# Kernel optimization log

Measured on AMD Instinct MI355X. Metric: run time of the kernel, lower is better.

## Reference

```python
import jax, jax.numpy as jnp
import numpy as np

N, E, IN, H, D = 20000, 640000, 256, 4, 32
NEG_SLOPE = 0.2


def setup_inputs() -> dict:
    key = jax.random.key(0)
    ks = jax.random.split(key, 8)
    feat = jax.random.normal(ks[0], (N, IN), dtype=jnp.float32)
    pr_score = jax.random.uniform(ks[1], (N,), dtype=jnp.float32) + 1e-3
    edge_src = jax.random.randint(ks[2], (E,), 0, N)
    edge_dst = jax.random.randint(ks[3], (E,), 0, N)
    # parameters (xavier-ish scale)
    fc_w = jax.random.normal(ks[4], (H * D, IN), dtype=jnp.float32) * (2.0 / np.sqrt(IN + H * D))
    attn_l = jax.random.normal(ks[5], (1, H, D), dtype=jnp.float32) * (2.0 / np.sqrt(1 + D))
    attn_r = jax.random.normal(ks[6], (1, H, D), dtype=jnp.float32) * (2.0 / np.sqrt(1 + D))
    bias = jnp.zeros((H * D,), dtype=jnp.float32)
    return {"feat": feat, "pr_score": pr_score, "edge_src": edge_src,
            "edge_dst": edge_dst, "fc_w": fc_w, "attn_l": attn_l,
            "attn_r": attn_r, "bias": bias}


def reference(feat, pr_score, edge_src, edge_dst, fc_w, attn_l, attn_r, bias):
    n = feat.shape[0]
    h, d = attn_l.shape[1], attn_l.shape[2]
    # feat_src = fc(feat).view(N, H, D)
    ft = (feat @ fc_w.T).reshape(n, h, d)                       # [N,H,D]
    el = jnp.sum(ft * attn_l, axis=-1)                          # [N,H]
    er = jnp.sum(ft * attn_r, axis=-1)                          # [N,H]
    e = jax.nn.leaky_relu(el[edge_src] + er[edge_dst], NEG_SLOPE)  # [E,H]
    # edge_softmax over incoming edges per destination node
    emax = jax.ops.segment_max(e, edge_dst, num_segments=n)
    ee = jnp.exp(e - emax[edge_dst])
    esum = jax.ops.segment_sum(ee, edge_dst, num_segments=n)
    a = ee / esum[edge_dst]                                     # [E,H]
    # PageRank-style normalization: b = pr[src] / sum_{in-edges}(pr[src])
    pr_src = pr_score[edge_src]                                 # [E]
    pr_sum = jax.ops.segment_sum(pr_src, edge_dst, num_segments=n)
    b = pr_src / pr_sum[edge_dst]                               # [E]
    c = a * b[:, None]                                          # [E,H]
    csum = jax.ops.segment_sum(c, edge_dst, num_segments=n)
    c = c / csum[edge_dst]                                      # [E,H]
    # weighted aggregation: rst[dst] = sum_e ft[src_e] * c_e
    m = ft[edge_src] * c[:, :, None]                            # [E,H,D]
    rst = jax.ops.segment_sum(m, edge_dst, num_segments=n)      # [N,H,D]
    rst = rst + bias.reshape(1, h, d)
    return rst
```

## Files before the change

kernel.cpp:

```cpp
#include <hip/hip_runtime.h>

#define IN_DIM 256
#define HD 128
#define NHEAD 4
#define NEG_SLOPE 0.2f
#define ELLW 128

typedef unsigned int  uint;
typedef unsigned short ushort_t;

typedef short bf16x8 __attribute__((ext_vector_type(8)));
typedef float f32x4  __attribute__((ext_vector_type(4)));

__device__ __forceinline__ ushort_t f2bf(float x) {
    uint u = __float_as_uint(x);
    u += 0x7fffu + ((u >> 16) & 1u);
    return (ushort_t)(u >> 16);
}
__device__ __forceinline__ uint pack2(float lo, float hi) {
    return (uint)f2bf(lo) | ((uint)f2bf(hi) << 16);
}
__device__ __forceinline__ float bflo(uint u) { return __uint_as_float(u << 16); }
__device__ __forceinline__ float bfhi(uint u) { return __uint_as_float(u & 0xffff0000u); }

#define GBM 64
#define GBK 64
#define LDK 72

__global__ __launch_bounds__(256) void gemm_mfma(
    const float* __restrict__ feat, const float* __restrict__ fcw,
    const float* __restrict__ attn_l, const float* __restrict__ attn_r,
    const float* __restrict__ pr,
    ushort_t* __restrict__ ft16, float* __restrict__ elp, float* __restrict__ er,
    int* __restrict__ deg, int n)
{
    __shared__ ushort_t s_a[GBM * LDK];
    __shared__ ushort_t s_b[64 * LDK];

    const int t = threadIdx.x;
    {
        const int z = blockIdx.x * 256 + t;
        if (z < n) deg[z] = 0;
    }

    const int tile = blockIdx.x >> 1;
    const int half = blockIdx.x & 1;
    const int row0 = tile * GBM;
    const int col0 = half * 64;
    const int w    = t >> 6;
    const int lane = t & 63;
    const int fr   = lane & 15;
    const int fq   = lane >> 4;

    f32x4 acc[4];
#pragma unroll
    for (int nt = 0; nt < 4; ++nt) acc[nt] = (f32x4){0.f, 0.f, 0.f, 0.f};

    const int s_row = t >> 2, s_kca = (t & 3) * 16;
    const int s_col = t >> 2, s_kcb = (t & 3) * 16;

    const ushort_t* pa  = &s_a[(w * 16 + fr) * LDK + fq * 8];
    const ushort_t* pb0 = &s_b[fr * LDK + fq * 8];

    for (int k0 = 0; k0 < IN_DIM; k0 += GBK) {
        {
            const int grow = row0 + s_row;
            float4 v0, v1, v2, v3;
            if (grow < n) {
                const float* p = feat + (size_t)grow * IN_DIM + k0 + s_kca;
                v0 = *(const float4*)(p + 0);
                v1 = *(const float4*)(p + 4);
                v2 = *(const float4*)(p + 8);
                v3 = *(const float4*)(p + 12);
            } else {
                v0 = make_float4(0.f,0.f,0.f,0.f); v1 = v0; v2 = v0; v3 = v0;
            }
            uint4* dst = (uint4*)&s_a[s_row * LDK + s_kca];
            dst[0] = make_uint4(pack2(v0.x,v0.y), pack2(v0.z,v0.w),
                                pack2(v1.x,v1.y), pack2(v1.z,v1.w));
            dst[1] = make_uint4(pack2(v2.x,v2.y), pack2(v2.z,v2.w),
                                pack2(v3.x,v3.y), pack2(v3.z,v3.w));
        }
        {
            const float* p = fcw + (size_t)(col0 + s_col) * IN_DIM + k0 + s_kcb;
            float4 u0 = *(const float4*)(p + 0);
            float4 u1 = *(const float4*)(p + 4);
            float4 u2 = *(const float4*)(p + 8);
            float4 u3 = *(const float4*)(p + 12);
            uint4* dst = (uint4*)&s_b[s_col * LDK + s_kcb];
            dst[0] = make_uint4(pack2(u0.x,u0.y), pack2(u0.z,u0.w),
                                pack2(u1.x,u1.y), pack2(u1.z,u1.w));
            dst[1] = make_uint4(pack2(u2.x,u2.y), pack2(u2.z,u2.w),
                                pack2(u3.x,u3.y), pack2(u3.z,u3.w));
        }
        __syncthreads();

        const bf16x8 a0 = *(const bf16x8*)pa;
        const bf16x8 a1 = *(const bf16x8*)(pa + 32);
#pragma unroll
        for (int nt = 0; nt < 4; ++nt) {
            const ushort_t* pb = pb0 + nt * 16 * LDK;
            const bf16x8 b0 = *(const bf16x8*)pb;
            const bf16x8 b1 = *(const bf16x8*)(pb + 32);
            acc[nt] = __builtin_amdgcn_mfma_f32_16x16x32_bf16(a0, b0, acc[nt], 0, 0, 0);
            acc[nt] = __builtin_amdgcn_mfma_f32_16x16x32_bf16(a1, b1, acc[nt], 0, 0, 0);
        }
        __syncthreads();
    }

    const int h0 = 2 * half;
    float al[4], ar_[4];
#pragma unroll
    for (int nt = 0; nt < 4; ++nt) {
        al[nt]  = attn_l[col0 + nt * 16 + fr];
        ar_[nt] = attn_r[col0 + nt * 16 + fr];
    }

#pragma unroll
    for (int j = 0; j < 4; ++j) {
        const int grow = row0 + w * 16 + fq * 4 + j;
        const bool ok = grow < n;
        if (ok) {
#pragma unroll
            for (int nt = 0; nt < 4; ++nt)
                ft16[(size_t)grow * HD + col0 + nt * 16 + fr] = f2bf(acc[nt][j]);
        }
        float plA = acc[0][j]*al[0] + acc[1][j]*al[1];
        float plB = acc[2][j]*al[2] + acc[3][j]*al[3];
        float peA = acc[0][j]*ar_[0] + acc[1][j]*ar_[1];
        float peB = acc[2][j]*ar_[2] + acc[3][j]*ar_[3];
#pragma unroll
        for (int m = 1; m < 16; m <<= 1) {
            plA += __shfl_xor(plA, m, 64); plB += __shfl_xor(plB, m, 64);
            peA += __shfl_xor(peA, m, 64); peB += __shfl_xor(peB, m, 64);
        }
        if (ok && fr == 0) {
            *(float2*)&elp[(size_t)grow * 8 + h0] = make_float2(plA, plB);
            *(float2*)&er[(size_t)grow * NHEAD + h0] = make_float2(peA, peB);
            if (half == 0) elp[(size_t)grow * 8 + 4] = pr[grow];
        }
    }
}

__global__ void build_ell(const int* __restrict__ src, const int* __restrict__ dst,
                          int* __restrict__ deg, int* __restrict__ ell, int e)
{
    int i = blockIdx.x * blockDim.x + threadIdx.x;
    if (i < e) {
        const int d = dst[i];
        const int r = atomicAdd(&deg[d], 1);
        if (r < ELLW) ell[(size_t)d * ELLW + r] = src[i];
    }
}

__global__ __launch_bounds__(256) void aggregate(
    const uint4* __restrict__ ftu4, const float* __restrict__ elp,
    const float* __restrict__ er,
    const int* __restrict__ deg, const int* __restrict__ ell,
    const float* __restrict__ bias, float* __restrict__ out, int n)
{
    const int wave = threadIdx.x >> 6;
    const int lane = threadIdx.x & 63;
    const int slot = lane >> 4;
    const int sub  = lane & 15;
    const int head = sub >> 2;
    const int dst  = blockIdx.x * 4 + wave;

    __shared__ float s_w[4][NHEAD][72];
    __shared__ int   s_s[4][72];

    if (dst >= n) return;

    if (lane < 8) {
        s_s[wave][64 + lane] = 0;
#pragma unroll
        for (int hh = 0; hh < NHEAD; ++hh) s_w[wave][hh][64 + lane] = 0.f;
    }

    const int dg  = min(deg[dst], ELLW);
    const int beg = dst * ELLW;
    const float4 e4 = *(const float4*)&er[(size_t)dst * NHEAD];

    float aA[8], aB[8];
#pragma unroll
    for (int i = 0; i < 8; ++i) { aA[i] = 0.f; aB[i] = 0.f; }
    float wS = 0.f;

    for (int base = 0; base < dg; base += 64) {
        const int len = min(64, dg - base);
        if (lane < len) {
            const int s = ell[beg + base + lane];
            const float4 l4 = *(const float4*)&elp[(size_t)s * 8];
            const float p   = elp[(size_t)s * 8 + 4];
            float e0 = l4.x + e4.x, e1 = l4.y + e4.y;
            float e2 = l4.z + e4.z, e3 = l4.w + e4.w;
            e0 = e0 > 0.f ? e0 : NEG_SLOPE * e0;
            e1 = e1 > 0.f ? e1 : NEG_SLOPE * e1;
            e2 = e2 > 0.f ? e2 : NEG_SLOPE * e2;
            e3 = e3 > 0.f ? e3 : NEG_SLOPE * e3;
            s_w[wave][0][lane] = __expf(e0) * p;
            s_w[wave][1][lane] = __expf(e1) * p;
            s_w[wave][2][lane] = __expf(e2) * p;
            s_w[wave][3][lane] = __expf(e3) * p;
            s_s[wave][lane] = s;
        } else {
            s_w[wave][0][lane] = 0.f; s_w[wave][1][lane] = 0.f;
            s_w[wave][2][lane] = 0.f; s_w[wave][3][lane] = 0.f;
            s_s[wave][lane] = 0;
        }
        for (int j = 0; j < len; j += 8) {
            const int eA = j + slot;
            const int eB = j + 4 + slot;
            const int   sA = s_s[wave][eA];
            const int   sB = s_s[wave][eB];
            const float wA = s_w[wave][head][eA];
            const float wB = s_w[wave][head][eB];
            const uint4 uA = ftu4[(size_t)sA * 16 + sub];
            const uint4 uB = ftu4[(size_t)sB * 16 + sub];
            wS += wA + wB;
            aA[0] = fmaf(wA, bflo(uA.x), aA[0]);
            aA[1] = fmaf(wA, bfhi(uA.x), aA[1]);
            aA[2] = fmaf(wA, bflo(uA.y), aA[2]);
            aA[3] = fmaf(wA, bfhi(uA.y), aA[3]);
            aA[4] = fmaf(wA, bflo(uA.z), aA[4]);
            aA[5] = fmaf(wA, bfhi(uA.z), aA[5]);
            aA[6] = fmaf(wA, bflo(uA.w), aA[6]);
            aA[7] = fmaf(wA, bfhi(uA.w), aA[7]);
            aB[0] = fmaf(wB, bflo(uB.x), aB[0]);
            aB[1] = fmaf(wB, bfhi(uB.x), aB[1]);
            aB[2] = fmaf(wB, bflo(uB.y), aB[2]);
            aB[3] = fmaf(wB, bfhi(uB.y), aB[3]);
            aB[4] = fmaf(wB, bflo(uB.z), aB[4]);
            aB[5] = fmaf(wB, bfhi(uB.z), aB[5]);
            aB[6] = fmaf(wB, bflo(uB.w), aB[6]);
            aB[7] = fmaf(wB, bfhi(uB.w), aB[7]);
        }
    }

    float a[8];
#pragma unroll
    for (int i = 0; i < 8; ++i) a[i] = aA[i] + aB[i];
#pragma unroll
    for (int i = 0; i < 8; ++i) {
        a[i] += __shfl_xor(a[i], 16, 64);
        a[i] += __shfl_xor(a[i], 32, 64);
    }
    wS += __shfl_xor(wS, 16, 64);
    wS += __shfl_xor(wS, 32, 64);

    if (slot == 0) {
        const float inv = (dg > 0) ? 1.f / wS : 0.f;
        const float4 b0 = *(const float4*)&bias[8 * sub];
        const float4 b1 = *(const float4*)&bias[8 * sub + 4];
        float4 r0, r1;
        r0.x = a[0] * inv + b0.x; r0.y = a[1] * inv + b0.y;
        r0.z = a[2] * inv + b0.z; r0.w = a[3] * inv + b0.w;
        r1.x = a[4] * inv + b1.x; r1.y = a[5] * inv + b1.y;
        r1.z = a[6] * inv + b1.z; r1.w = a[7] * inv + b1.w;
        *(float4*)&out[(size_t)dst * HD + 8 * sub]     = r0;
        *(float4*)&out[(size_t)dst * HD + 8 * sub + 4] = r1;
    }
}

extern "C" void kernel_launch(void* const* d_in, const int* in_sizes, int n_in,
                              void* d_out, int out_size, void* d_ws, size_t ws_size,
                              hipStream_t stream)
{
    const float* feat   = (const float*)d_in[0];
    const float* pr     = (const float*)d_in[1];
    const int*   esrc   = (const int*)d_in[2];
    const int*   edst   = (const int*)d_in[3];
    const float* fcw    = (const float*)d_in[4];
    const float* attn_l = (const float*)d_in[5];
    const float* attn_r = (const float*)d_in[6];
    const float* bias   = (const float*)d_in[7];
    float* out = (float*)d_out;

    const int n = in_sizes[0] / IN_DIM;
    const int e = in_sizes[2];

    char* ws = (char*)d_ws;
    size_t off = 0;
    auto wsalloc = [&](size_t bytes) -> void* {
        void* p = ws + off;
        off += (bytes + 255) & ~(size_t)255;
        return p;
    };
    ushort_t* ft16 = (ushort_t*)wsalloc((size_t)n * HD * sizeof(ushort_t));
    float* elp  = (float*)wsalloc((size_t)n * 8 * sizeof(float));
    float* er   = (float*)wsalloc((size_t)n * NHEAD * sizeof(float));
    int*   deg  = (int*)wsalloc((size_t)n * sizeof(int));
    int*   ell  = (int*)wsalloc((size_t)n * ELLW * sizeof(int));

    const int ntiles = (n + GBM - 1) / GBM;
    gemm_mfma<<<2 * ntiles, 256, 0, stream>>>(feat, fcw, attn_l, attn_r, pr,
                                              ft16, elp, er, deg, n);
    build_ell<<<(e + 255) / 256, 256, 0, stream>>>(esrc, edst, deg, ell, e);
    aggregate<<<(n + 3) / 4, 256, 0, stream>>>((const uint4*)ft16, elp, er,
                                               deg, ell, bias, out, n);
}
```

Before: 74.36 us.

## Fuse GEMM, ELL build and aggregation into one cooperative persistent kernel

```diff
diff --git a/kernel.cpp b/kernel.cpp
--- a/kernel.cpp
+++ b/kernel.cpp
@@ -1,10 +1,18 @@
 #include <hip/hip_runtime.h>
+#include <hip/hip_cooperative_groups.h>
+
+namespace cg = cooperative_groups;
 
 #define IN_DIM 256
 #define HD 128
 #define NHEAD 4
 #define NEG_SLOPE 0.2f
 #define ELLW 128
+#define GBM 64
+#define GBK 64
+#define LDK 72
+#define GRIDF 512
+#define G_GEMM 352
 
 typedef unsigned int  uint;
 typedef unsigned short ushort_t;
@@ -23,28 +31,17 @@
 __device__ __forceinline__ float bflo(uint u) { return __uint_as_float(u << 16); }
 __device__ __forceinline__ float bfhi(uint u) { return __uint_as_float(u & 0xffff0000u); }
 
-#define GBM 64
-#define GBK 64
-#define LDK 72
-
-__global__ __launch_bounds__(256) void gemm_mfma(
+__device__ __forceinline__ void gemm_half(
+    ushort_t* __restrict__ s_a, ushort_t* __restrict__ s_b, int tile2,
     const float* __restrict__ feat, const float* __restrict__ fcw,
     const float* __restrict__ attn_l, const float* __restrict__ attn_r,
     const float* __restrict__ pr,
     ushort_t* __restrict__ ft16, float* __restrict__ elp, float* __restrict__ er,
-    int* __restrict__ deg, int n)
-{
-    __shared__ ushort_t s_a[GBM * LDK];
-    __shared__ ushort_t s_b[64 * LDK];
-
-    const int t = threadIdx.x;
-    {
-        const int z = blockIdx.x * 256 + t;
-        if (z < n) deg[z] = 0;
-    }
-
-    const int tile = blockIdx.x >> 1;
-    const int half = blockIdx.x & 1;
+    int n)
+{
+    const int t    = threadIdx.x;
+    const int tile = tile2 >> 1;
+    const int half = tile2 & 1;
     const int row0 = tile * GBM;
     const int col0 = half * 64;
     const int w    = t >> 6;
@@ -56,8 +53,7 @@
 #pragma unroll
     for (int nt = 0; nt < 4; ++nt) acc[nt] = (f32x4){0.f, 0.f, 0.f, 0.f};
 
-    const int s_row = t >> 2, s_kca = (t & 3) * 16;
-    const int s_col = t >> 2, s_kcb = (t & 3) * 16;
+    const int s_row = t >> 2, s_kc = (t & 3) * 16;
 
     const ushort_t* pa  = &s_a[(w * 16 + fr) * LDK + fq * 8];
     const ushort_t* pb0 = &s_b[fr * LDK + fq * 8];
@@ -67,7 +63,7 @@
             const int grow = row0 + s_row;
             float4 v0, v1, v2, v3;
             if (grow < n) {
-                const float* p = feat + (size_t)grow * IN_DIM + k0 + s_kca;
+                const float* p = feat + (size_t)grow * IN_DIM + k0 + s_kc;
                 v0 = *(const float4*)(p + 0);
                 v1 = *(const float4*)(p + 4);
                 v2 = *(const float4*)(p + 8);
@@ -75,19 +71,19 @@
             } else {
                 v0 = make_float4(0.f,0.f,0.f,0.f); v1 = v0; v2 = v0; v3 = v0;
             }
-            uint4* dst = (uint4*)&s_a[s_row * LDK + s_kca];
+            uint4* dst = (uint4*)&s_a[s_row * LDK + s_kc];
             dst[0] = make_uint4(pack2(v0.x,v0.y), pack2(v0.z,v0.w),
                                 pack2(v1.x,v1.y), pack2(v1.z,v1.w));
             dst[1] = make_uint4(pack2(v2.x,v2.y), pack2(v2.z,v2.w),
                                 pack2(v3.x,v3.y), pack2(v3.z,v3.w));
         }
         {
-            const float* p = fcw + (size_t)(col0 + s_col) * IN_DIM + k0 + s_kcb;
+            const float* p = fcw + (size_t)(col0 + s_row) * IN_DIM + k0 + s_kc;
             float4 u0 = *(const float4*)(p + 0);
             float4 u1 = *(const float4*)(p + 4);
             float4 u2 = *(const float4*)(p + 8);
             float4 u3 = *(const float4*)(p + 12);
-            uint4* dst = (uint4*)&s_b[s_col * LDK + s_kcb];
+            uint4* dst = (uint4*)&s_b[s_row * LDK + s_kc];
             dst[0] = make_uint4(pack2(u0.x,u0.y), pack2(u0.z,u0.w),
                                 pack2(u1.x,u1.y), pack2(u1.z,u1.w));
             dst[1] = make_uint4(pack2(u2.x,u2.y), pack2(u2.z,u2.w),
@@ -142,40 +138,16 @@
     }
 }
 
-__global__ void build_ell(const int* __restrict__ src, const int* __restrict__ dst,
-                          int* __restrict__ deg, int* __restrict__ ell, int e)
-{
-    int i = blockIdx.x * blockDim.x + threadIdx.x;
-    if (i < e) {
-        const int d = dst[i];
-        const int r = atomicAdd(&deg[d], 1);
-        if (r < ELLW) ell[(size_t)d * ELLW + r] = src[i];
-    }
-}
-
-__global__ __launch_bounds__(256) void aggregate(
+__device__ __forceinline__ void agg_one(
     const uint4* __restrict__ ftu4, const float* __restrict__ elp,
     const float* __restrict__ er,
     const int* __restrict__ deg, const int* __restrict__ ell,
-    const float* __restrict__ bias, float* __restrict__ out, int n)
-{
-    const int wave = threadIdx.x >> 6;
-    const int lane = threadIdx.x & 63;
+    const float* __restrict__ bias, float* __restrict__ out,
+    int dst, int lane, float (*__restrict__ sw)[72], int* __restrict__ ss)
+{
     const int slot = lane >> 4;
     const int sub  = lane & 15;
     const int head = sub >> 2;
-    const int dst  = blockIdx.x * 4 + wave;
-
-    __shared__ float s_w[4][NHEAD][72];
-    __shared__ int   s_s[4][72];
-
-    if (dst >= n) return;
-
-    if (lane < 8) {
-        s_s[wave][64 + lane] = 0;
-#pragma unroll
-        for (int hh = 0; hh < NHEAD; ++hh) s_w[wave][hh][64 + lane] = 0.f;
-    }
 
     const int dg  = min(deg[dst], ELLW);
     const int beg = dst * ELLW;
@@ -198,23 +170,23 @@
             e1 = e1 > 0.f ? e1 : NEG_SLOPE * e1;
             e2 = e2 > 0.f ? e2 : NEG_SLOPE * e2;
             e3 = e3 > 0.f ? e3 : NEG_SLOPE * e3;
-            s_w[wave][0][lane] = __expf(e0) * p;
-            s_w[wave][1][lane] = __expf(e1) * p;
-            s_w[wave][2][lane] = __expf(e2) * p;
-            s_w[wave][3][lane] = __expf(e3) * p;
-            s_s[wave][lane] = s;
+            sw[0][lane] = __expf(e0) * p;
+            sw[1][lane] = __expf(e1) * p;
+            sw[2][lane] = __expf(e2) * p;
+            sw[3][lane] = __expf(e3) * p;
+            ss[lane] = s;
         } else {
-            s_w[wave][0][lane] = 0.f; s_w[wave][1][lane] = 0.f;
-            s_w[wave][2][lane] = 0.f; s_w[wave][3][lane] = 0.f;
-            s_s[wave][lane] = 0;
+            sw[0][lane] = 0.f; sw[1][lane] = 0.f;
+            sw[2][lane] = 0.f; sw[3][lane] = 0.f;
+            ss[lane] = 0;
         }
         for (int j = 0; j < len; j += 8) {
             const int eA = j + slot;
             const int eB = j + 4 + slot;
-            const int   sA = s_s[wave][eA];
-            const int   sB = s_s[wave][eB];
-            const float wA = s_w[wave][head][eA];
-            const float wB = s_w[wave][head][eB];
+            const int   sA = ss[eA];
+            const int   sB = ss[eB];
+            const float wA = sw[head][eA];
+            const float wB = sw[head][eB];
             const uint4 uA = ftu4[(size_t)sA * 16 + sub];
             const uint4 uB = ftu4[(size_t)sB * 16 + sub];
             wS += wA + wB;
@@ -262,6 +234,106 @@
     }
 }
 
+union SmemU {
+    struct { ushort_t a[GBM * LDK]; ushort_t b[64 * LDK]; } g;
+    struct { float w[4][NHEAD][72]; int s[4][72]; } agg;
+};
+
+__global__ void
+__attribute__((amdgpu_flat_work_group_size(256, 256), amdgpu_waves_per_eu(2, 2)))
+fused_all(
+    const float* __restrict__ feat, const float* __restrict__ pr,
+    const int* __restrict__ esrc, const int* __restrict__ edst,
+    const float* __restrict__ fcw, const float* __restrict__ attn_l,
+    const float* __restrict__ attn_r, const float* __restrict__ bias,
+    float* __restrict__ out, ushort_t* __restrict__ ft16,
+    float* __restrict__ elp, float* __restrict__ er,
+    int* __restrict__ deg, int* __restrict__ ell, int n, int e)
+{
+    __shared__ SmemU sm;
+    const int t = threadIdx.x;
+    cg::grid_group grid = cg::this_grid();
+
+    for (int i = blockIdx.x * 256 + t; i < n; i += GRIDF * 256) deg[i] = 0;
+    __threadfence();
+    grid.sync();
+
+    if (blockIdx.x < G_GEMM) {
+        const int ntiles2 = 2 * ((n + GBM - 1) / GBM);
+        for (int t2 = blockIdx.x; t2 < ntiles2; t2 += G_GEMM)
+            gemm_half(sm.g.a, sm.g.b, t2, feat, fcw, attn_l, attn_r, pr,
+                      ft16, elp, er, n);
+    } else {
+        const int stride = (GRIDF - G_GEMM) * 256;
+        for (int i = (blockIdx.x - G_GEMM) * 256 + t; i < e; i += stride) {
+            const int d = edst[i];
+            const int r = atomicAdd(&deg[d], 1);
+            if (r < ELLW) ell[(size_t)d * ELLW + r] = esrc[i];
+        }
+    }
+    __threadfence();
+    grid.sync();
+
+    const int wave = t >> 6;
+    const int lane = t & 63;
+    float (*sw)[72] = sm.agg.w[wave];
+    int* ss = sm.agg.s[wave];
+    if (lane < 8) {
+        ss[64 + lane] = 0;
+#pragma unroll
+        for (int hh = 0; hh < NHEAD; ++hh) sw[hh][64 + lane] = 0.f;
+    }
+    for (int dst = blockIdx.x * 4 + wave; dst < n; dst += GRIDF * 4)
+        agg_one((const uint4*)ft16, elp, er, deg, ell, bias, out,
+                dst, lane, sw, ss);
+}
+
+__global__ __launch_bounds__(256) void gemm_mfma_k(
+    const float* __restrict__ feat, const float* __restrict__ fcw,
+    const float* __restrict__ attn_l, const float* __restrict__ attn_r,
+    const float* __restrict__ pr,
+    ushort_t* __restrict__ ft16, float* __restrict__ elp, float* __restrict__ er,
+    int* __restrict__ deg, int n)
+{
+    __shared__ SmemU sm;
+    const int z = blockIdx.x * 256 + threadIdx.x;
+    if (z < n) deg[z] = 0;
+    gemm_half(sm.g.a, sm.g.b, blockIdx.x, feat, fcw, attn_l, attn_r, pr,
+              ft16, elp, er, n);
+}
+
+__global__ void build_ell_k(const int* __restrict__ src, const int* __restrict__ dst,
+                            int* __restrict__ deg, int* __restrict__ ell, int e)
+{
+    int i = blockIdx.x * blockDim.x + threadIdx.x;
+    if (i < e) {
+        const int d = dst[i];
+        const int r = atomicAdd(&deg[d], 1);
+        if (r < ELLW) ell[(size_t)d * ELLW + r] = src[i];
+    }
+}
+
+__global__ __launch_bounds__(256) void aggregate_k(
+    const uint4* __restrict__ ftu4, const float* __restrict__ elp,
+    const float* __restrict__ er,
+    const int* __restrict__ deg, const int* __restrict__ ell,
+    const float* __restrict__ bias, float* __restrict__ out, int n)
+{
+    __shared__ SmemU sm;
+    const int wave = threadIdx.x >> 6;
+    const int lane = threadIdx.x & 63;
+    float (*sw)[72] = sm.agg.w[wave];
+    int* ss = sm.agg.s[wave];
+    if (lane < 8) {
+        ss[64 + lane] = 0;
+#pragma unroll
+        for (int hh = 0; hh < NHEAD; ++hh) sw[hh][64 + lane] = 0.f;
+    }
+    const int dst = blockIdx.x * 4 + wave;
+    if (dst < n)
+        agg_one(ftu4, elp, er, deg, ell, bias, out, dst, lane, sw, ss);
+}
+
 extern "C" void kernel_launch(void* const* d_in, const int* in_sizes, int n_in,
                               void* d_out, int out_size, void* d_ws, size_t ws_size,
                               hipStream_t stream)
@@ -276,8 +348,8 @@
     const float* bias   = (const float*)d_in[7];
     float* out = (float*)d_out;
 
-    const int n = in_sizes[0] / IN_DIM;
-    const int e = in_sizes[2];
+    int n = in_sizes[0] / IN_DIM;
+    int e = in_sizes[2];
 
     char* ws = (char*)d_ws;
     size_t off = 0;
@@ -292,10 +364,17 @@
     int*   deg  = (int*)wsalloc((size_t)n * sizeof(int));
     int*   ell  = (int*)wsalloc((size_t)n * ELLW * sizeof(int));
 
-    const int ntiles = (n + GBM - 1) / GBM;
-    gemm_mfma<<<2 * ntiles, 256, 0, stream>>>(feat, fcw, attn_l, attn_r, pr,
-                                              ft16, elp, er, deg, n);
-    build_ell<<<(e + 255) / 256, 256, 0, stream>>>(esrc, edst, deg, ell, e);
-    aggregate<<<(n + 3) / 4, 256, 0, stream>>>((const uint4*)ft16, elp, er,
-                                               deg, ell, bias, out, n);
-}
+    void* args[] = { &feat, &pr, &esrc, &edst, &fcw, &attn_l, &attn_r, &bias,
+                     &out, &ft16, &elp, &er, &deg, &ell, &n, &e };
+    hipError_t cerr = hipLaunchCooperativeKernel(fused_all, dim3(GRIDF), dim3(256),
+                                                 args, 0, stream);
+    if (cerr != hipSuccess) {
+        (void)hipGetLastError();
+        const int ntiles2 = 2 * ((n + GBM - 1) / GBM);
+        gemm_mfma_k<<<ntiles2, 256, 0, stream>>>(feat, fcw, attn_l, attn_r, pr,
+                                                 ft16, elp, er, deg, n);
+        build_ell_k<<<(e + 255) / 256, 256, 0, stream>>>(esrc, edst, deg, ell, e);
+        aggregate_k<<<(n + 3) / 4, 256, 0, stream>>>((const uint4*)ft16, elp, er,
+                                                     deg, ell, bias, out, n);
+    }
+}
```

New measurement: 268.3 us. 261% more time.

## Compute edge attention weights in ELL build kernel instead of aggregate

Applied to the files above, without the earlier changes.

```diff
diff --git a/kernel.cpp b/kernel.cpp
--- a/kernel.cpp
+++ b/kernel.cpp
@@ -56,8 +56,7 @@
 #pragma unroll
     for (int nt = 0; nt < 4; ++nt) acc[nt] = (f32x4){0.f, 0.f, 0.f, 0.f};
 
-    const int s_row = t >> 2, s_kca = (t & 3) * 16;
-    const int s_col = t >> 2, s_kcb = (t & 3) * 16;
+    const int s_row = t >> 2, s_kc = (t & 3) * 16;
 
     const ushort_t* pa  = &s_a[(w * 16 + fr) * LDK + fq * 8];
     const ushort_t* pb0 = &s_b[fr * LDK + fq * 8];
@@ -67,7 +66,7 @@
             const int grow = row0 + s_row;
             float4 v0, v1, v2, v3;
             if (grow < n) {
-                const float* p = feat + (size_t)grow * IN_DIM + k0 + s_kca;
+                const float* p = feat + (size_t)grow * IN_DIM + k0 + s_kc;
                 v0 = *(const float4*)(p + 0);
                 v1 = *(const float4*)(p + 4);
                 v2 = *(const float4*)(p + 8);
@@ -75,19 +74,19 @@
             } else {
                 v0 = make_float4(0.f,0.f,0.f,0.f); v1 = v0; v2 = v0; v3 = v0;
             }
-            uint4* dst = (uint4*)&s_a[s_row * LDK + s_kca];
+            uint4* dst = (uint4*)&s_a[s_row * LDK + s_kc];
             dst[0] = make_uint4(pack2(v0.x,v0.y), pack2(v0.z,v0.w),
                                 pack2(v1.x,v1.y), pack2(v1.z,v1.w));
             dst[1] = make_uint4(pack2(v2.x,v2.y), pack2(v2.z,v2.w),
                                 pack2(v3.x,v3.y), pack2(v3.z,v3.w));
         }
         {
-            const float* p = fcw + (size_t)(col0 + s_col) * IN_DIM + k0 + s_kcb;
+            const float* p = fcw + (size_t)(col0 + s_row) * IN_DIM + k0 + s_kc;
             float4 u0 = *(const float4*)(p + 0);
             float4 u1 = *(const float4*)(p + 4);
             float4 u2 = *(const float4*)(p + 8);
             float4 u3 = *(const float4*)(p + 12);
-            uint4* dst = (uint4*)&s_b[s_col * LDK + s_kcb];
+            uint4* dst = (uint4*)&s_b[s_row * LDK + s_kc];
             dst[0] = make_uint4(pack2(u0.x,u0.y), pack2(u0.z,u0.w),
                                 pack2(u1.x,u1.y), pack2(u1.z,u1.w));
             dst[1] = make_uint4(pack2(u2.x,u2.y), pack2(u2.z,u2.w),
@@ -142,21 +141,42 @@
     }
 }
 
-__global__ void build_ell(const int* __restrict__ src, const int* __restrict__ dst,
-                          int* __restrict__ deg, int* __restrict__ ell, int e)
+__global__ void build_ell_w(
+    const int* __restrict__ src, const int* __restrict__ dst,
+    const float* __restrict__ elp, const float* __restrict__ er,
+    int* __restrict__ deg, int* __restrict__ ell_src,
+    float4* __restrict__ ell_w, int e)
 {
     int i = blockIdx.x * blockDim.x + threadIdx.x;
-    if (i < e) {
-        const int d = dst[i];
-        const int r = atomicAdd(&deg[d], 1);
-        if (r < ELLW) ell[(size_t)d * ELLW + r] = src[i];
-    }
+    if (i >= e) return;
+    const int d = dst[i];
+    const int s = src[i];
+    const int r = atomicAdd(&deg[d], 1);
+    if (r >= ELLW) return;
+
+    const float4 l4 = *(const float4*)&elp[(size_t)s * 8];
+    const float p   = elp[(size_t)s * 8 + 4];
+    const float4 e4 = *(const float4*)&er[(size_t)d * NHEAD];
+    float e0 = l4.x + e4.x, e1 = l4.y + e4.y;
+    float e2 = l4.z + e4.z, e3 = l4.w + e4.w;
+    e0 = e0 > 0.f ? e0 : NEG_SLOPE * e0;
+    e1 = e1 > 0.f ? e1 : NEG_SLOPE * e1;
+    e2 = e2 > 0.f ? e2 : NEG_SLOPE * e2;
+    e3 = e3 > 0.f ? e3 : NEG_SLOPE * e3;
+    float4 w4;
+    w4.x = __expf(e0) * p;
+    w4.y = __expf(e1) * p;
+    w4.z = __expf(e2) * p;
+    w4.w = __expf(e3) * p;
+    const size_t slot = (size_t)d * ELLW + r;
+    ell_src[slot] = s;
+    ell_w[slot]   = w4;
 }
 
 __global__ __launch_bounds__(256) void aggregate(
-    const uint4* __restrict__ ftu4, const float* __restrict__ elp,
-    const float* __restrict__ er,
-    const int* __restrict__ deg, const int* __restrict__ ell,
+    const uint4* __restrict__ ftu4,
+    const int* __restrict__ deg, const int* __restrict__ ell_src,
+    const float4* __restrict__ ell_w,
     const float* __restrict__ bias, float* __restrict__ out, int n)
 {
     const int wave = threadIdx.x >> 6;
@@ -179,7 +199,6 @@
 
     const int dg  = min(deg[dst], ELLW);
     const int beg = dst * ELLW;
-    const float4 e4 = *(const float4*)&er[(size_t)dst * NHEAD];
 
     float aA[8], aB[8];
 #pragma unroll
@@ -189,19 +208,10 @@
     for (int base = 0; base < dg; base += 64) {
         const int len = min(64, dg - base);
         if (lane < len) {
-            const int s = ell[beg + base + lane];
-            const float4 l4 = *(const float4*)&elp[(size_t)s * 8];
-            const float p   = elp[(size_t)s * 8 + 4];
-            float e0 = l4.x + e4.x, e1 = l4.y + e4.y;
-            float e2 = l4.z + e4.z, e3 = l4.w + e4.w;
-            e0 = e0 > 0.f ? e0 : NEG_SLOPE * e0;
-            e1 = e1 > 0.f ? e1 : NEG_SLOPE * e1;
-            e2 = e2 > 0.f ? e2 : NEG_SLOPE * e2;
-            e3 = e3 > 0.f ? e3 : NEG_SLOPE * e3;
-            s_w[wave][0][lane] = __expf(e0) * p;
-            s_w[wave][1][lane] = __expf(e1) * p;
-            s_w[wave][2][lane] = __expf(e2) * p;
-            s_w[wave][3][lane] = __expf(e3) * p;
+            const int   s  = ell_src[beg + base + lane];
+            const float4 w4 = ell_w[beg + base + lane];
+            s_w[wave][0][lane] = w4.x; s_w[wave][1][lane] = w4.y;
+            s_w[wave][2][lane] = w4.z; s_w[wave][3][lane] = w4.w;
             s_s[wave][lane] = s;
         } else {
             s_w[wave][0][lane] = 0.f; s_w[wave][1][lane] = 0.f;
@@ -286,16 +296,18 @@
         off += (bytes + 255) & ~(size_t)255;
         return p;
     };
-    ushort_t* ft16 = (ushort_t*)wsalloc((size_t)n * HD * sizeof(ushort_t));
-    float* elp  = (float*)wsalloc((size_t)n * 8 * sizeof(float));
-    float* er   = (float*)wsalloc((size_t)n * NHEAD * sizeof(float));
-    int*   deg  = (int*)wsalloc((size_t)n * sizeof(int));
-    int*   ell  = (int*)wsalloc((size_t)n * ELLW * sizeof(int));
-
-    const int ntiles = (n + GBM - 1) / GBM;
-    gemm_mfma<<<2 * ntiles, 256, 0, stream>>>(feat, fcw, attn_l, attn_r, pr,
-                                              ft16, elp, er, deg, n);
-    build_ell<<<(e + 255) / 256, 256, 0, stream>>>(esrc, edst, deg, ell, e);
-    aggregate<<<(n + 3) / 4, 256, 0, stream>>>((const uint4*)ft16, elp, er,
-                                               deg, ell, bias, out, n);
-}
+    ushort_t* ft16   = (ushort_t*)wsalloc((size_t)n * HD * sizeof(ushort_t));
+    float*    elp    = (float*)wsalloc((size_t)n * 8 * sizeof(float));
+    float*    er     = (float*)wsalloc((size_t)n * NHEAD * sizeof(float));
+    int*      deg    = (int*)wsalloc((size_t)n * sizeof(int));
+    int*      ellsrc = (int*)wsalloc((size_t)n * ELLW * sizeof(int));
+    float4*   ellw   = (float4*)wsalloc((size_t)n * ELLW * sizeof(float4));
+
+    const int ntiles2 = 2 * ((n + GBM - 1) / GBM);
+    gemm_mfma<<<ntiles2, 256, 0, stream>>>(feat, fcw, attn_l, attn_r, pr,
+                                           ft16, elp, er, deg, n);
+    build_ell_w<<<(e + 255) / 256, 256, 0, stream>>>(esrc, edst, elp, er,
+                                                     deg, ellsrc, ellw, e);
+    aggregate<<<(n + 3) / 4, 256, 0, stream>>>((const uint4*)ft16,
+                                               deg, ellsrc, ellw, bias, out, n);
+}
```

New measurement: 78.80 us. +6.0%, slower.

## Run ELL build concurrently with GEMM in one fused launch

Applied to the files above, without the earlier changes.

```diff
diff --git a/kernel.cpp b/kernel.cpp
--- a/kernel.cpp
+++ b/kernel.cpp
@@ -27,21 +27,35 @@
 #define GBK 64
 #define LDK 72
 
-__global__ __launch_bounds__(256) void gemm_mfma(
+__global__ void zero_deg(int* __restrict__ deg, int n)
+{
+    int i = blockIdx.x * blockDim.x + threadIdx.x;
+    if (i < n) deg[i] = 0;
+}
+
+__global__ __launch_bounds__(256) void gemm_and_ell(
     const float* __restrict__ feat, const float* __restrict__ fcw,
     const float* __restrict__ attn_l, const float* __restrict__ attn_r,
     const float* __restrict__ pr,
+    const int* __restrict__ esrc, const int* __restrict__ edst,
     ushort_t* __restrict__ ft16, float* __restrict__ elp, float* __restrict__ er,
-    int* __restrict__ deg, int n)
+    int* __restrict__ deg, int* __restrict__ ell,
+    int n, int e, int ntiles2)
 {
+    const int t = threadIdx.x;
+
+    if (blockIdx.x >= ntiles2) {
+        const int i = (blockIdx.x - ntiles2) * 256 + t;
+        if (i < e) {
+            const int d = edst[i];
+            const int r = atomicAdd(&deg[d], 1);
+            if (r < ELLW) ell[(size_t)d * ELLW + r] = esrc[i];
+        }
+        return;
+    }
+
     __shared__ ushort_t s_a[GBM * LDK];
     __shared__ ushort_t s_b[64 * LDK];
-
-    const int t = threadIdx.x;
-    {
-        const int z = blockIdx.x * 256 + t;
-        if (z < n) deg[z] = 0;
-    }
 
     const int tile = blockIdx.x >> 1;
     const int half = blockIdx.x & 1;
@@ -56,8 +70,7 @@
 #pragma unroll
     for (int nt = 0; nt < 4; ++nt) acc[nt] = (f32x4){0.f, 0.f, 0.f, 0.f};
 
-    const int s_row = t >> 2, s_kca = (t & 3) * 16;
-    const int s_col = t >> 2, s_kcb = (t & 3) * 16;
+    const int s_row = t >> 2, s_kc = (t & 3) * 16;
 
     const ushort_t* pa  = &s_a[(w * 16 + fr) * LDK + fq * 8];
     const ushort_t* pb0 = &s_b[fr * LDK + fq * 8];
@@ -67,7 +80,7 @@
             const int grow = row0 + s_row;
             float4 v0, v1, v2, v3;
             if (grow < n) {
-                const float* p = feat + (size_t)grow * IN_DIM + k0 + s_kca;
+                const float* p = feat + (size_t)grow * IN_DIM + k0 + s_kc;
                 v0 = *(const float4*)(p + 0);
                 v1 = *(const float4*)(p + 4);
                 v2 = *(const float4*)(p + 8);
@@ -75,19 +88,19 @@
             } else {
                 v0 = make_float4(0.f,0.f,0.f,0.f); v1 = v0; v2 = v0; v3 = v0;
             }
-            uint4* dst = (uint4*)&s_a[s_row * LDK + s_kca];
+            uint4* dst = (uint4*)&s_a[s_row * LDK + s_kc];
             dst[0] = make_uint4(pack2(v0.x,v0.y), pack2(v0.z,v0.w),
                                 pack2(v1.x,v1.y), pack2(v1.z,v1.w));
             dst[1] = make_uint4(pack2(v2.x,v2.y), pack2(v2.z,v2.w),
                                 pack2(v3.x,v3.y), pack2(v3.z,v3.w));
         }
         {
-            const float* p = fcw + (size_t)(col0 + s_col) * IN_DIM + k0 + s_kcb;
+            const float* p = fcw + (size_t)(col0 + s_row) * IN_DIM + k0 + s_kc;
             float4 u0 = *(const float4*)(p + 0);
             float4 u1 = *(const float4*)(p + 4);
             float4 u2 = *(const float4*)(p + 8);
             float4 u3 = *(const float4*)(p + 12);
-            uint4* dst = (uint4*)&s_b[s_col * LDK + s_kcb];
+            uint4* dst = (uint4*)&s_b[s_row * LDK + s_kc];
             dst[0] = make_uint4(pack2(u0.x,u0.y), pack2(u0.z,u0.w),
                                 pack2(u1.x,u1.y), pack2(u1.z,u1.w));
             dst[1] = make_uint4(pack2(u2.x,u2.y), pack2(u2.z,u2.w),
@@ -139,17 +152,6 @@
             *(float2*)&er[(size_t)grow * NHEAD + h0] = make_float2(peA, peB);
             if (half == 0) elp[(size_t)grow * 8 + 4] = pr[grow];
         }
-    }
-}
-
-__global__ void build_ell(const int* __restrict__ src, const int* __restrict__ dst,
-                          int* __restrict__ deg, int* __restrict__ ell, int e)
-{
-    int i = blockIdx.x * blockDim.x + threadIdx.x;
-    if (i < e) {
-        const int d = dst[i];
-        const int r = atomicAdd(&deg[d], 1);
-        if (r < ELLW) ell[(size_t)d * ELLW + r] = src[i];
     }
 }
 
@@ -292,10 +294,13 @@
     int*   deg  = (int*)wsalloc((size_t)n * sizeof(int));
     int*   ell  = (int*)wsalloc((size_t)n * ELLW * sizeof(int));
 
-    const int ntiles = (n + GBM - 1) / GBM;
-    gemm_mfma<<<2 * ntiles, 256, 0, stream>>>(feat, fcw, attn_l, attn_r, pr,
-                                              ft16, elp, er, deg, n);
-    build_ell<<<(e + 255) / 256, 256, 0, stream>>>(esrc, edst, deg, ell, e);
+    const int ntiles2 = 2 * ((n + GBM - 1) / GBM);
+    const int eblocks = (e + 255) / 256;
+
+    zero_deg<<<(n + 255) / 256, 256, 0, stream>>>(deg, n);
+    gemm_and_ell<<<ntiles2 + eblocks, 256, 0, stream>>>(
+        feat, fcw, attn_l, attn_r, pr, esrc, edst,
+        ft16, elp, er, deg, ell, n, e, ntiles2);
     aggregate<<<(n + 3) / 4, 256, 0, stream>>>((const uint4*)ft16, elp, er,
                                                deg, ell, bias, out, n);
 }
```

New measurement: 75.48 us. Within noise of the previous version (+1.5%).
